# Optimization experiments

Hardware: AMD Instinct MI355X
Metric: run time of the kernel (lower is better)

## Reference

```python
import jax, jax.numpy as jnp
import numpy as np

HEADS = 4
PK = 32  # patch_kernel


def _starts(size, step, d):
    out = []
    for i in range(0, size + step - d, step):
        out.append(min(i, size - d))
    return np.asarray(out)


def dwconv3(x, w, b=None):
    # depthwise 3x3 conv, NCHW, weight (C,1,3,3)
    y = jax.lax.conv_general_dilated(
        x, w, window_strides=(1, 1), padding=((1, 1), (1, 1)),
        dimension_numbers=("NCHW", "OIHW", "NCHW"), feature_group_count=x.shape[1])
    if b is not None:
        y = y + b[None, :, None, None]
    return y


def conv1(x, w):
    # 1x1 conv as channel matmul, weight (O, C)
    return jnp.einsum("bchw,oc->bohw", x, w)


def partition(x, step, d):
    # overlapping windows, matching local_partition (i outer, j inner)
    b, c, h, w = x.shape
    sh = _starts(h, step, d)
    sw = _starts(w, step, d)
    ridx = sh[:, None] + np.arange(d)            # (nh, d)
    cidx = sw[:, None] + np.arange(d)            # (nw, d)
    xw = x[:, :, ridx, :]                        # (b, c, nh, d, w)
    xw = xw[:, :, :, :, cidx]                    # (b, c, nh, d, nw, d)
    xw = jnp.transpose(xw, (0, 2, 4, 1, 3, 5))   # (b, nh, nw, c, d, d)
    return xw.reshape(b, len(sh) * len(sw), c, d, d)


def reverse(shape, win, step, d):
    # overlap-add + count-based averaging, matching local_reverse
    b, c, h, w = shape
    sh = _starts(h, step, d)
    sw = _starts(w, step, d)
    nh, nw = len(sh), len(sw)
    ridx = (sh[:, None] + np.arange(d)).reshape(nh, 1, d, 1)
    cidx = (sw[:, None] + np.arange(d)).reshape(1, nw, 1, d)
    win6 = win.reshape(b, nh, nw, c, d, d).transpose(0, 3, 1, 2, 4, 5)  # (b,c,nh,nw,d,d)
    out = jnp.zeros(shape, win.dtype).at[:, :, ridx, cidx].add(win6)
    cnt = jnp.zeros((h, w), win.dtype).at[ridx, cidx].add(1.0)
    return out / cnt[None, None]


def setup_inputs() -> dict:
    key = jax.random.key(0)
    ks = jax.random.split(key, 9)
    b, dim, Hs, Hx = 2, 128, 62, 248
    s = 0.05
    return {
        "x": jax.random.normal(ks[0], (b, dim, Hx, Hx), jnp.float32),
        "sp": jax.random.normal(ks[1], (b, dim, Hs, Hs), jnp.float32),
        "w_pos": jax.random.normal(ks[2], (dim, 1, 3, 3), jnp.float32) * s,
        "b_pos": jax.random.normal(ks[3], (dim,), jnp.float32) * s,
        "w_q": jax.random.normal(ks[4], (dim, dim), jnp.float32) * s,
        "w_qdw": jax.random.normal(ks[5], (dim, 1, 3, 3), jnp.float32) * s,
        "w_kv": jax.random.normal(ks[6], (2 * dim, dim), jnp.float32) * s,
        "w_kvdw": jax.random.normal(ks[7], (2 * dim, 1, 3, 3), jnp.float32) * s,
        "w_out": jax.random.normal(ks[8], (dim, dim), jnp.float32) * s,
    }


def reference(x, sp, w_pos, b_pos, w_q, w_qdw, w_kv, w_kvdw, w_out):
    p1, p2 = PK, PK // 4               # 32, 8
    s1, s2 = p1 - p1 // 4, p2 - p2 // 4  # 24, 6
    x = x + dwconv3(x, w_pos, b_pos)
    sp = sp + dwconv3(sp, w_pos, b_pos)
    q = dwconv3(conv1(sp, w_q), w_qdw)      # (b, c, Hs, Ws)
    kv = dwconv3(conv1(x, w_kv), w_kvdw)    # (b, 2c, Hx, Wx)
    qw = partition(q, s2, p2)               # (b, n, c, 8, 8)
    kvw = partition(kv, s1, p1)             # (b, n, 2c, 32, 32)
    kw, vw = jnp.split(kvw, 2, axis=2)
    b, n, c = qw.shape[0], qw.shape[1], qw.shape[2]
    hd = c // HEADS

    def to_heads(t, d):  # 'b n (head c) dh dw -> (b n) head (dh dw) c'
        return t.reshape(b * n, HEADS, hd, d * d).transpose(0, 1, 3, 2)

    qh, kh, vh = to_heads(qw, p2), to_heads(kw, p1), to_heads(vw, p1)
    attn = jax.nn.softmax(jnp.einsum("bhqc,bhkc->bhqk", qh, kh) * (hd ** -0.5), axis=-1)
    out = jnp.einsum("bhqk,bhkc->bhqc", attn, vh)
    out = out.transpose(0, 1, 3, 2).reshape(b, n, c, p2, p2)
    out = reverse(sp.shape, out, s2, p2)
    return conv1(out, w_out)
```

## Files before the change

### kernel.cpp

```cpp
#include <hip/hip_runtime.h>
#include <cstdint>

#define HS 62
#define HX 248
#define HXW (HX * HX)
#define HSW (HS * HS)
#define HXP 256
#define HXWP (HX * HXP)

typedef __attribute__((ext_vector_type(8))) short bf16x8;
typedef __attribute__((ext_vector_type(4))) float f32x4;
typedef __attribute__((ext_vector_type(2))) float f32x2;

static __device__ __forceinline__ unsigned short f2bf(float f) {
  uint32_t u = __builtin_bit_cast(uint32_t, f);
  u += 0x7fff + ((u >> 16) & 1);
  return (unsigned short)(u >> 16);
}
static __device__ __forceinline__ float bf2f(unsigned short u) {
  uint32_t x = (uint32_t)u << 16;
  return __builtin_bit_cast(float, x);
}
static __device__ __forceinline__ float bflo(uint32_t u) {
  return __builtin_bit_cast(float, u << 16);
}
static __device__ __forceinline__ float bfhi(uint32_t u) {
  return __builtin_bit_cast(float, u & 0xffff0000u);
}

static __device__ __forceinline__ void pkfma(f32x2& acc, f32x2 a, f32x2 b) {
  asm("v_pk_fma_f32 %0, %1, %2, %0" : "+v"(acc) : "v"(a), "v"(b));
}
static __device__ __forceinline__ uint32_t cvtpk(float lo, float hi) {
  uint32_t r;
  asm("v_cvt_pk_bf16_f32 %0, %1, %2" : "=v"(r) : "v"(lo), "v"(hi));
  return r;
}
static __device__ __forceinline__ f32x2 unp(uint32_t u) {
  f32x2 r;
  r.x = __builtin_bit_cast(float, u << 16);
  r.y = __builtin_bit_cast(float, u & 0xffff0000u);
  return r;
}

__global__ void dwconv3_kernel(const float* __restrict__ x, const float* __restrict__ w,
                               const float* __restrict__ bias, float* __restrict__ y,
                               int C, int H, int W, int total, int residual) {
  int i = blockIdx.x * 256 + threadIdx.x;
  if (i >= total) return;
  int wx = i % W;
  int t = i / W;
  int hy = t % H;
  int bc = t / H;
  int c = bc % C;
  const float* xb = x + (size_t)bc * H * W;
  const float* wc = w + c * 9;
  float s = bias ? bias[c] : 0.0f;
  for (int di = -1; di <= 1; di++) {
    int h2 = hy + di;
    if (h2 < 0 || h2 >= H) continue;
    for (int dj = -1; dj <= 1; dj++) {
      int w2 = wx + dj;
      if (w2 < 0 || w2 >= W) continue;
      s += xb[(size_t)h2 * W + w2] * wc[(di + 1) * 3 + (dj + 1)];
    }
  }
  if (residual) s += xb[(size_t)hy * W + wx];
  y[i] = s;
}

__global__ __launch_bounds__(256) void dwconv8x2_bf16_kernel(
    const float* __restrict__ x, const float* __restrict__ w,
    const float* __restrict__ bias, unsigned short* __restrict__ y, int total) {
  int i = blockIdx.x * 256 + threadIdx.x;
  if (i >= total) return;
  int wq = (i % 31) * 8;
  int t = i / 31;
  int hp = t % 124;
  int bc = t / 124;
  int c = bc & 127;
  int hy = hp * 2;
  const float* xb = x + (size_t)bc * HXW;
  const float* wc = w + c * 9;
  float bv = bias[c];

  float rm1[10], r0[10], r1[10], r2[10];
  auto loadrow = [&](int h2, float (&r)[10]) {
    const float* row = xb + (size_t)h2 * HX + wq;
    float4 a = *(const float4*)row;
    float4 b2 = *(const float4*)(row + 4);
    r[1] = a.x;  r[2] = a.y;  r[3] = a.z;  r[4] = a.w;
    r[5] = b2.x; r[6] = b2.y; r[7] = b2.z; r[8] = b2.w;
    r[0] = (wq > 0) ? row[-1] : 0.0f;
    r[9] = (wq + 8 < HX) ? row[8] : 0.0f;
  };
  loadrow((hy > 0) ? hy - 1 : 0, rm1);
  loadrow(hy, r0);
  loadrow(hy + 1, r1);
  loadrow((hy + 2 < HX) ? hy + 2 : HX - 1, r2);
  if (hp == 0) {
#pragma unroll
    for (int k = 0; k < 10; k++) rm1[k] = 0.0f;
  }
  if (hp == 123) {
#pragma unroll
    for (int k = 0; k < 10; k++) r2[k] = 0.0f;
  }

  float w0 = wc[0], w1 = wc[1], w2 = wc[2];
  float w3 = wc[3], w4 = wc[4], w5 = wc[5];
  float w6 = wc[6], w7 = wc[7], w8 = wc[8];

  float o0[8], o1[8];
#pragma unroll
  for (int k = 0; k < 8; k++) {
    float s = bv;
    s += w0 * rm1[k]; s += w1 * rm1[k + 1]; s += w2 * rm1[k + 2];
    s += w3 * r0[k];  s += w4 * r0[k + 1];  s += w5 * r0[k + 2];
    s += w6 * r1[k];  s += w7 * r1[k + 1];  s += w8 * r1[k + 2];
    o0[k] = s + r0[k + 1];
    float u = bv;
    u += w0 * r0[k]; u += w1 * r0[k + 1]; u += w2 * r0[k + 2];
    u += w3 * r1[k]; u += w4 * r1[k + 1]; u += w5 * r1[k + 2];
    u += w6 * r2[k]; u += w7 * r2[k + 1]; u += w8 * r2[k + 2];
    o1[k] = u + r1[k + 1];
  }
  uint4 d0, d1;
  d0.x = cvtpk(o0[0], o0[1]); d0.y = cvtpk(o0[2], o0[3]);
  d0.z = cvtpk(o0[4], o0[5]); d0.w = cvtpk(o0[6], o0[7]);
  d1.x = cvtpk(o1[0], o1[1]); d1.y = cvtpk(o1[2], o1[3]);
  d1.z = cvtpk(o1[4], o1[5]); d1.w = cvtpk(o1[6], o1[7]);
  unsigned short* yb = y + (size_t)bc * HXW + (size_t)hy * HX + wq;
  *(uint4*)yb = d0;
  *(uint4*)(yb + HX) = d1;
}

__global__ void cvt_bf16_kernel(const float* __restrict__ src, unsigned short* __restrict__ dst,
                                int n) {
  int i = blockIdx.x * 256 + threadIdx.x;
  if (i < n) dst[i] = f2bf(src[i]);
}

__global__ void dwconv_q_kernel(const float* __restrict__ x, const float* __restrict__ w,
                                unsigned short* __restrict__ qn, int total) {
  int i = blockIdx.x * 256 + threadIdx.x;
  if (i >= total) return;
  int wx = i % HS;
  int t = i / HS;
  int hy = t % HS;
  int bc = t / HS;
  int c = bc & 127;
  int b = bc >> 7;
  const float* xb = x + (size_t)bc * HSW;
  const float* wc = w + c * 9;
  float s = 0.0f;
  for (int di = -1; di <= 1; di++) {
    int h2 = hy + di;
    if (h2 < 0 || h2 >= HS) continue;
    for (int dj = -1; dj <= 1; dj++) {
      int w2 = wx + dj;
      if (w2 < 0 || w2 >= HS) continue;
      s += xb[(size_t)h2 * HS + w2] * wc[(di + 1) * 3 + (dj + 1)];
    }
  }
  qn[((size_t)(b * HSW + hy * HS + wx)) * 128 + c] = f2bf(s * 0.17677669529663688f);
}

__global__ __launch_bounds__(256) void conv1_kv_mfma_kernel(
    const unsigned short* __restrict__ xpb,
    const unsigned short* __restrict__ wkb,
    unsigned short* __restrict__ y) {
  int b = blockIdx.y;
  int p0 = blockIdx.x * 64;
  int tid = threadIdx.x;
  int wave = tid >> 6, lane = tid & 63, quad = lane >> 4, l15 = lane & 15;
  __shared__ __align__(16) unsigned short bufA[64 * 136];
  __shared__ __align__(16) unsigned short bufW[64 * 136];

  {
    int c = tid >> 1, half = tid & 1;
    const unsigned short* src = xpb + ((size_t)(b * 128 + c)) * HXW + p0 + half * 32;
#pragma unroll
    for (int j = 0; j < 8; j++) {
      uint2 v = *(const uint2*)(src + j * 4);
      int px = half * 32 + j * 4;
      bufA[(px + 0) * 136 + c] = (unsigned short)(v.x & 0xffff);
      bufA[(px + 1) * 136 + c] = (unsigned short)(v.x >> 16);
      bufA[(px + 2) * 136 + c] = (unsigned short)(v.y & 0xffff);
      bufA[(px + 3) * 136 + c] = (unsigned short)(v.y >> 16);
    }
  }
  __syncthreads();
  bf16x8 A[4];
#pragma unroll
  for (int kb = 0; kb < 4; kb++)
    A[kb] = __builtin_bit_cast(bf16x8,
        *(const uint4*)&bufA[(wave * 16 + l15) * 136 + kb * 32 + quad * 8]);

  const f32x4 zf = {0.f, 0.f, 0.f, 0.f};
#pragma unroll 1
  for (int h = 0; h < 2; h++) {
#pragma unroll 1
    for (int oq = 0; oq < 2; oq++) {
      __syncthreads();
      {
        int orow = tid >> 2;
        int cseg = (tid & 3) * 32;
        const unsigned short* src = wkb + (size_t)(h * 128 + oq * 64 + orow) * 128 + cseg;
        unsigned short* dst = &bufW[orow * 136 + cseg];
        *(uint4*)(dst)      = *(const uint4*)(src);
        *(uint4*)(dst + 8)  = *(const uint4*)(src + 8);
        *(uint4*)(dst + 16) = *(const uint4*)(src + 16);
        *(uint4*)(dst + 24) = *(const uint4*)(src + 24);
      }
      __syncthreads();
#pragma unroll
      for (int ot = 0; ot < 4; ot++) {
        const unsigned short* wrow = &bufW[(ot * 16 + l15) * 136 + quad * 8];
        f32x4 D = zf;
        D = __builtin_amdgcn_mfma_f32_16x16x32_bf16(A[0], __builtin_bit_cast(bf16x8, *(const uint4*)(wrow)),      D, 0, 0, 0);
        D = __builtin_amdgcn_mfma_f32_16x16x32_bf16(A[1], __builtin_bit_cast(bf16x8, *(const uint4*)(wrow + 32)), D, 0, 0, 0);
        D = __builtin_amdgcn_mfma_f32_16x16x32_bf16(A[2], __builtin_bit_cast(bf16x8, *(const uint4*)(wrow + 64)), D, 0, 0, 0);
        D = __builtin_amdgcn_mfma_f32_16x16x32_bf16(A[3], __builtin_bit_cast(bf16x8, *(const uint4*)(wrow + 96)), D, 0, 0, 0);
#pragma unroll
        for (int r = 0; r < 4; r++)
          bufA[(wave * 16 + quad * 4 + r) * 136 + (oq * 4 + ot) * 16 + l15] = f2bf(D[r]);
      }
    }
    __syncthreads();
    {
      int px = tid >> 2, og = (tid & 3) * 32;
      const uint4* srcp = (const uint4*)&bufA[px * 136 + og];
      uint4* dstp = (uint4*)(y + ((size_t)b * HXW + p0 + px) * 256 + h * 128 + og);
#pragma unroll
      for (int j = 0; j < 4; j++) dstp[j] = srcp[j];
    }
  }
}

template <bool VT, bool VB>
static __device__ __forceinline__ void dwkv_rowpair(
    const unsigned short* __restrict__ rm1, const unsigned short* __restrict__ r0,
    const unsigned short* __restrict__ r1, const unsigned short* __restrict__ r2,
    const f32x2 (&wp)[9], int px0, f32x2 (&a0)[8], f32x2 (&a1)[8]) {
  const f32x2 z2 = {0.f, 0.f};
#pragma unroll
  for (int p = 0; p < 8; p++) { a0[p] = z2; a1[p] = z2; }
#pragma unroll
  for (int j = 0; j < 10; j++) {
    int xcol = px0 - 1 + j;
    int xc = xcol;
    if (j == 0) xc = (xcol < 0) ? 0 : xcol;
    if (j == 9) xc = (xcol > HX - 1) ? HX - 1 : xcol;
    size_t off = (size_t)xc * 256;
    uint32_t um1 = 0, u0, u1, u2 = 0;
    u0 = *(const uint32_t*)(r0 + off);
    u1 = *(const uint32_t*)(r1 + off);
    if constexpr (VT) um1 = *(const uint32_t*)(rm1 + off);
    if constexpr (VB) u2 = *(const uint32_t*)(r2 + off);
    if (j == 0 || j == 9) {
      bool oob = (j == 0) ? (xcol < 0) : (xcol > HX - 1);
      if (oob) { um1 = 0u; u0 = 0u; u1 = 0u; u2 = 0u; }
    }
    f32x2 dm1, d0 = unp(u0), d1 = unp(u1), d2;
    if constexpr (VT) dm1 = unp(um1);
    if constexpr (VB) d2 = unp(u2);
    if (j <= 7) {
      if constexpr (VT) pkfma(a0[j], wp[0], dm1);
      pkfma(a0[j], wp[3], d0);
      pkfma(a0[j], wp[6], d1);
      pkfma(a1[j], wp[0], d0);
      pkfma(a1[j], wp[3], d1);
      if constexpr (VB) pkfma(a1[j], wp[6], d2);
    }
    if (j >= 1 && j <= 8) {
      if constexpr (VT) pkfma(a0[j - 1], wp[1], dm1);
      pkfma(a0[j - 1], wp[4], d0);
      pkfma(a0[j - 1], wp[7], d1);
      pkfma(a1[j - 1], wp[1], d0);
      pkfma(a1[j - 1], wp[4], d1);
      if constexpr (VB) pkfma(a1[j - 1], wp[7], d2);
    }
    if (j >= 2) {
      if constexpr (VT) pkfma(a0[j - 2], wp[2], dm1);
      pkfma(a0[j - 2], wp[5], d0);
      pkfma(a0[j - 2], wp[8], d1);
      pkfma(a1[j - 2], wp[2], d0);
      pkfma(a1[j - 2], wp[5], d1);
      if constexpr (VB) pkfma(a1[j - 2], wp[8], d2);
    }
  }
}

#define VTS 72
#define VTROW (128 * VTS + 16)

__global__ __launch_bounds__(512) __attribute__((amdgpu_waves_per_eu(4)))
void dwconv_kv_kernel(const unsigned short* __restrict__ tkv,
                      const float* __restrict__ w,
                      unsigned short* __restrict__ kT,
                      unsigned short* __restrict__ vv) {
  int fid = blockIdx.x;
  int xcd = fid & 7, slot = fid >> 3;
  int gi = xcd * 62 + slot;
  int strip = gi / 124;
  int g = gi % 124;
  int b = blockIdx.y;
  int x0 = strip * 64;
  int tid = threadIdx.x;
  int cl = tid & 127;
  int pg = tid >> 7;
  int ch0 = cl * 2;
  int hy0 = g * 2;

  f32x2 wp[9];
#pragma unroll
  for (int t = 0; t < 9; t++) {
    wp[t].x = w[ch0 * 9 + t];
    wp[t].y = w[(ch0 + 1) * 9 + t];
  }

  __shared__ __align__(16) unsigned short vt[2 * VTROW];

  const unsigned short* r0 = tkv + (size_t)b * HXW * 256 + (size_t)hy0 * (HX * 256) + ch0;
  const unsigned short* r1 = r0 + HX * 256;
  const unsigned short* rm1 = r0 - HX * 256;
  const unsigned short* r2 = r1 + HX * 256;
  bool isK = (cl < 64);
  int c0 = ch0 - 128;

#pragma unroll 1
  for (int half = 0; half < 2; half++) {
    int px0 = x0 + pg * 16 + half * 8;
    if (px0 < HX) {
      f32x2 a0[8], a1[8];
      if (g == 0)        dwkv_rowpair<false, true >(rm1, r0, r1, r2, wp, px0, a0, a1);
      else if (g == 123) dwkv_rowpair<true,  false>(rm1, r0, r1, r2, wp, px0, a0, a1);
      else               dwkv_rowpair<true,  true >(rm1, r0, r1, r2, wp, px0, a0, a1);

      if (isK) {
        unsigned short* kb0 = kT + ((size_t)b * HXW + (size_t)hy0 * HX + px0) * 128 + ch0;
        unsigned short* kb1 = kb0 + (size_t)HX * 128;
#pragma unroll
        for (int p = 0; p < 8; p++) {
          *(uint32_t*)(kb0 + (size_t)p * 128) = cvtpk(a0[p].x, a0[p].y);
          *(uint32_t*)(kb1 + (size_t)p * 128) = cvtpk(a1[p].x, a1[p].y);
        }
      } else {
        int pxr = pg * 16 + half * 8;
        unsigned short* v0 = vt + c0 * VTS + pxr;
        unsigned short* v1 = v0 + VTS;
        uint2 d;
        d.x = cvtpk(a0[0].x, a0[1].x); d.y = cvtpk(a0[2].x, a0[3].x);
        *(uint2*)(v0) = d;
        d.x = cvtpk(a0[4].x, a0[5].x); d.y = cvtpk(a0[6].x, a0[7].x);
        *(uint2*)(v0 + 4) = d;
        d.x = cvtpk(a0[0].y, a0[1].y); d.y = cvtpk(a0[2].y, a0[3].y);
        *(uint2*)(v1) = d;
        d.x = cvtpk(a0[4].y, a0[5].y); d.y = cvtpk(a0[6].y, a0[7].y);
        *(uint2*)(v1 + 4) = d;
        d.x = cvtpk(a1[0].x, a1[1].x); d.y = cvtpk(a1[2].x, a1[3].x);
        *(uint2*)(v0 + VTROW) = d;
        d.x = cvtpk(a1[4].x, a1[5].x); d.y = cvtpk(a1[6].x, a1[7].x);
        *(uint2*)(v0 + VTROW + 4) = d;
        d.x = cvtpk(a1[0].y, a1[1].y); d.y = cvtpk(a1[2].y, a1[3].y);
        *(uint2*)(v1 + VTROW) = d;
        d.x = cvtpk(a1[4].y, a1[5].y); d.y = cvtpk(a1[6].y, a1[7].y);
        *(uint2*)(v1 + VTROW + 4) = d;
      }
    }
  }
  __syncthreads();
  {
    int ch = tid >> 2;
    int row = (tid >> 1) & 1;
    int ph = (tid & 1) * 32;
    const unsigned short* srcv = vt + row * VTROW + ch * VTS + ph;
    unsigned short* dst = vv + (size_t)(b * 128 + ch) * HXWP + (size_t)(hy0 + row) * HXP + x0 + ph;
#pragma unroll
    for (int j = 0; j < 4; j++)
      *(uint4*)(dst + j * 8) = *(const uint4*)(srcv + j * 8);
  }
}

template <int O>
__global__ __launch_bounds__(256) void conv1_kernel(const float* __restrict__ x,
                                                    const float* __restrict__ w,
                                                    float* __restrict__ y, int HW) {
  constexpr int K = 128;
  constexpr int BK = 32;
  __shared__ __align__(16) float ws_s[BK][64];
  __shared__ __align__(16) float xs_s[BK][64];
  int b = blockIdx.z;
  int o0 = blockIdx.y * 64;
  int p0 = blockIdx.x * 64;
  const float* xb = x + (size_t)b * K * HW;
  int tx = threadIdx.x & 15;
  int ty = threadIdx.x >> 4;
  float acc[4][4] = {};
  int lo = threadIdx.x >> 2;
  int lk = (threadIdx.x & 3) * 8;
  int lc = threadIdx.x >> 3;
  int lp = (threadIdx.x & 7) * 8;

  for (int k0 = 0; k0 < K; k0 += BK) {
    __syncthreads();
    {
      const float* wp = w + (size_t)(o0 + lo) * K + k0 + lk;
      float4 a = *(const float4*)wp;
      float4 bq = *(const float4*)(wp + 4);
      ws_s[lk + 0][lo] = a.x;  ws_s[lk + 1][lo] = a.y;
      ws_s[lk + 2][lo] = a.z;  ws_s[lk + 3][lo] = a.w;
      ws_s[lk + 4][lo] = bq.x; ws_s[lk + 5][lo] = bq.y;
      ws_s[lk + 6][lo] = bq.z; ws_s[lk + 7][lo] = bq.w;
    }
    {
      int p = p0 + lp;
      const float* xp = xb + (size_t)(k0 + lc) * HW;
      float4 a, bq;
      if (p + 7 < HW) {
        a = *(const float4*)(xp + p);
        bq = *(const float4*)(xp + p + 4);
      } else {
        float tv[8];
#pragma unroll
        for (int j = 0; j < 8; j++) tv[j] = (p + j < HW) ? xp[p + j] : 0.0f;
        a = make_float4(tv[0], tv[1], tv[2], tv[3]);
        bq = make_float4(tv[4], tv[5], tv[6], tv[7]);
      }
      *(float4*)&xs_s[lc][lp] = a;
      *(float4*)&xs_s[lc][lp + 4] = bq;
    }
    __syncthreads();
#pragma unroll
    for (int k = 0; k < BK; k++) {
      float4 wv = *(const float4*)&ws_s[k][ty * 4];
      float4 xv = *(const float4*)&xs_s[k][tx * 4];
      acc[0][0] += wv.x * xv.x; acc[0][1] += wv.x * xv.y; acc[0][2] += wv.x * xv.z; acc[0][3] += wv.x * xv.w;
      acc[1][0] += wv.y * xv.x; acc[1][1] += wv.y * xv.y; acc[1][2] += wv.y * xv.z; acc[1][3] += wv.y * xv.w;
      acc[2][0] += wv.z * xv.x; acc[2][1] += wv.z * xv.y; acc[2][2] += wv.z * xv.z; acc[2][3] += wv.z * xv.w;
      acc[3][0] += wv.w * xv.x; acc[3][1] += wv.w * xv.y; acc[3][2] += wv.w * xv.z; acc[3][3] += wv.w * xv.w;
    }
  }
  int p = p0 + tx * 4;
  float* yb = y + (size_t)b * O * HW + (size_t)(o0 + ty * 4) * HW;
#pragma unroll
  for (int j = 0; j < 4; j++) {
    float* yr = yb + (size_t)j * HW + p;
    if (p + 3 < HW) {
      *(float4*)yr = make_float4(acc[j][0], acc[j][1], acc[j][2], acc[j][3]);
    } else {
#pragma unroll
      for (int e = 0; e < 4; e++) if (p + e < HW) yr[e] = acc[j][e];
    }
  }
}

__global__ __launch_bounds__(256) void attn_mfma_kernel(
    const unsigned short* __restrict__ qn,
    const unsigned short* __restrict__ kT,
    const unsigned short* __restrict__ vp,
    float* __restrict__ o) {
  int fid = blockIdx.x;
  int xcd = fid & 7, slot = fid >> 3;
  int lin = xcd * 100 + slot;
  int n = lin % 100;
  int bh = lin / 100;
  int h = bh & 3, b = bh >> 2;
  int wi = n / 10, wj = n % 10;
  int wave = threadIdx.x >> 6;
  int oct = wave;
  int lane = threadIdx.x & 63;
  int quad = lane >> 4;
  int l15 = lane & 15;
  int y0 = 24 * wi, x0 = 24 * wj;

  __shared__ __align__(16) unsigned short lds[16896];
  unsigned short* Pw = lds + wave * 2560;

  bf16x8 QB[4];
#pragma unroll
  for (int nt = 0; nt < 4; nt++) {
    int qq = nt * 16 + l15;
    int qy = 6 * wi + (qq >> 3), qx = 6 * wj + (qq & 7);
    QB[nt] = __builtin_bit_cast(bf16x8,
        *(const uint4*)(qn + ((size_t)(b * HSW + qy * HS + qx)) * 128 + h * 32 + quad * 8));
  }

  f32x4 Oacc[2][4];
#pragma unroll
  for (int a = 0; a < 2; a++)
#pragma unroll
    for (int c = 0; c < 4; c++) Oacc[a][c] = f32x4{0.f, 0.f, 0.f, 0.f};
  float lsum[4] = {0.f, 0.f, 0.f, 0.f};

  const unsigned short* kb = kT + (size_t)b * HXW * 128 + h * 32;
  const unsigned short* vb = vp + ((size_t)(b * 128 + h * 32)) * HXWP;
  const f32x4 zf = {0.f, 0.f, 0.f, 0.f};

#define LOADROW(r, K0, K1, V0, V1)                                              \
  {                                                                             \
    int y = y0 + (r);                                                           \
    const unsigned short* krow = kb + ((size_t)(y * HX + x0)) * 128;            \
    K0 = *(const uint4*)(krow + (size_t)l15 * 128 + quad * 8);                  \
    K1 = *(const uint4*)(krow + (size_t)(16 + l15) * 128 + quad * 8);           \
    const unsigned short* vrow = vb + (size_t)y * HXP + x0 + quad * 8;          \
    V0 = *(const uint4*)(vrow + (size_t)l15 * HXWP);                            \
    V1 = *(const uint4*)(vrow + (size_t)(16 + l15) * HXWP);                     \
  }

  auto compute = [&](uint4 k0, uint4 k1, uint4 v0, uint4 v1) {
    bf16x8 KA0 = __builtin_bit_cast(bf16x8, k0);
    bf16x8 KA1 = __builtin_bit_cast(bf16x8, k1);
    bf16x8 VA0 = __builtin_bit_cast(bf16x8, v0);
    bf16x8 VA1 = __builtin_bit_cast(bf16x8, v1);
    f32x4 S[2][4];
#pragma unroll
    for (int nt = 0; nt < 4; nt++) {
      S[0][nt] = __builtin_amdgcn_mfma_f32_16x16x32_bf16(KA0, QB[nt], zf, 0, 0, 0);
      S[1][nt] = __builtin_amdgcn_mfma_f32_16x16x32_bf16(KA1, QB[nt], zf, 0, 0, 0);
    }
#pragma unroll
    for (int nt = 0; nt < 4; nt++) {
      float pv[2][4];
      float cs = 0.f;
#pragma unroll
      for (int mt = 0; mt < 2; mt++)
#pragma unroll
        for (int r = 0; r < 4; r++) {
          pv[mt][r] = __expf(S[mt][nt][r]);
          cs += pv[mt][r];
        }
      lsum[nt] += cs;
#pragma unroll
      for (int mt = 0; mt < 2; mt++) {
        uint2 d;
        d.x = (uint32_t)f2bf(pv[mt][0]) | ((uint32_t)f2bf(pv[mt][1]) << 16);
        d.y = (uint32_t)f2bf(pv[mt][2]) | ((uint32_t)f2bf(pv[mt][3]) << 16);
        *(uint2*)(Pw + (16 * nt + l15) * 40 + 16 * mt + quad * 4) = d;
      }
    }
#pragma unroll
    for (int nt = 0; nt < 4; nt++) {
      bf16x8 PB = __builtin_bit_cast(bf16x8, *(const uint4*)(Pw + (16 * nt + l15) * 40 + quad * 8));
      Oacc[0][nt] = __builtin_amdgcn_mfma_f32_16x16x32_bf16(VA0, PB, Oacc[0][nt], 0, 0, 0);
      Oacc[1][nt] = __builtin_amdgcn_mfma_f32_16x16x32_bf16(VA1, PB, Oacc[1][nt], 0, 0, 0);
    }
  };

  int rbase = oct * 8;
  uint4 kA0, kA1, vA0, vA1, kB0, kB1, vB0, vB1;
  LOADROW(rbase + 0, kA0, kA1, vA0, vA1);
  LOADROW(rbase + 1, kB0, kB1, vB0, vB1);
#pragma unroll 1
  for (int r = 0; r < 8; r += 2) {
    compute(kA0, kA1, vA0, vA1);
    {
      int rn = (r + 2 < 8) ? (r + 2) : 6;
      LOADROW(rbase + rn, kA0, kA1, vA0, vA1);
    }
    compute(kB0, kB1, vB0, vB1);
    {
      int rn = (r + 3 < 8) ? (r + 3) : 7;
      LOADROW(rbase + rn, kB0, kB1, vB0, vB1);
    }
  }
#undef LOADROW

#pragma unroll
  for (int nt = 0; nt < 4; nt++) {
    lsum[nt] += __shfl_xor(lsum[nt], 16, 64);
    lsum[nt] += __shfl_xor(lsum[nt], 32, 64);
  }

  float* mO = (float*)lds;
  float* mL = (float*)(lds + 16384);
  __syncthreads();
#pragma unroll
  for (int mt = 0; mt < 2; mt++)
#pragma unroll
    for (int nt = 0; nt < 4; nt++)
#pragma unroll
      for (int r = 0; r < 4; r++)
        mO[oct * 2048 + (16 * mt + quad * 4 + r) * 64 + 16 * nt + l15] = Oacc[mt][nt][r];
  if (quad == 0) {
#pragma unroll
    for (int nt = 0; nt < 4; nt++) mL[oct * 64 + nt * 16 + l15] = lsum[nt];
  }
  __syncthreads();
  {
    int q = threadIdx.x & 63;
    int cg = threadIdx.x >> 6;
    float inv = 1.0f / (mL[q] + mL[64 + q] + mL[128 + q] + mL[192 + q]);
    float* ob = o + (((size_t)(b * 100 + n)) * 128 + h * 32 + cg * 8) * 64 + q;
#pragma unroll
    for (int e = 0; e < 8; e++) {
      int ch = cg * 8 + e;
      float s = mO[ch * 64 + q] + mO[2048 + ch * 64 + q] +
                mO[4096 + ch * 64 + q] + mO[6144 + ch * 64 + q];
      ob[(size_t)e * 64] = s * inv;
    }
  }
}

__global__ void reverse_kernel(const float* __restrict__ win, float* __restrict__ out) {
  int i = blockIdx.x * 256 + threadIdx.x;
  const int total = 2 * 128 * HSW;
  if (i >= total) return;
  int x = i % HS;
  int t = i / HS;
  int y = t % HS;
  t /= HS;
  int c = t % 128;
  int b = t / 128;
  int wi0 = (y >= 7) ? (y - 2) / 6 : 0;
  int wi1 = min(9, y / 6);
  int wj0 = (x >= 7) ? (x - 2) / 6 : 0;
  int wj1 = min(9, x / 6);
  float s = 0.0f;
  for (int wi = wi0; wi <= wi1; wi++)
    for (int wj = wj0; wj <= wj1; wj++) {
      int di = y - 6 * wi, dj = x - 6 * wj;
      s += win[(((size_t)(b * 100 + wi * 10 + wj)) * 128 + c) * 64 + di * 8 + dj];
    }
  float cnt = (float)((wi1 - wi0 + 1) * (wj1 - wj0 + 1));
  out[i] = s / cnt;
}

extern "C" void kernel_launch(void* const* d_in, const int* in_sizes, int n_in,
                              void* d_out, int out_size, void* d_ws, size_t ws_size,
                              hipStream_t stream) {
  const float* x      = (const float*)d_in[0];
  const float* sp     = (const float*)d_in[1];
  const float* w_pos  = (const float*)d_in[2];
  const float* b_pos  = (const float*)d_in[3];
  const float* w_q    = (const float*)d_in[4];
  const float* w_qdw  = (const float*)d_in[5];
  const float* w_kv   = (const float*)d_in[6];
  const float* w_kvdw = (const float*)d_in[7];
  const float* w_out  = (const float*)d_in[8];
  float* out = (float*)d_out;

  const size_t N_x   = (size_t)2 * 128 * HXW;
  const size_t N_vp  = (size_t)2 * 128 * HXWP;
  const size_t N_s   = (size_t)2 * 128 * HSW;
  const size_t N_att = (size_t)2 * 100 * 128 * 64;

  float* ws = (float*)d_ws;
  unsigned short* xpb = (unsigned short*)ws;
  unsigned short* kT  = (unsigned short*)ws;
  unsigned short* vv  = kT + N_x;
  unsigned short* tkv = vv + N_vp;
  float* att = (float*)tkv;
  float* rev = att + N_att;
  float* spp = (float*)(tkv + 2 * N_x);
  float* tq  = spp + N_s;
  unsigned short* qn  = (unsigned short*)(tq + N_s);
  unsigned short* wkb = qn + N_s;
  (void)ws_size; (void)in_sizes; (void)n_in; (void)out_size;

  cvt_bf16_kernel<<<128, 256, 0, stream>>>(w_kv, wkb, 256 * 128);
  {
    int total = 2 * 128 * 124 * 31;
    dwconv8x2_bf16_kernel<<<(total + 255) / 256, 256, 0, stream>>>(x, w_pos, b_pos, xpb, total);
  }
  {
    int total = (int)N_s;
    dwconv3_kernel<<<(total + 255) / 256, 256, 0, stream>>>(sp, w_pos, b_pos, spp, 128, HS, HS, total, 1);
  }
  {
    int HW = HSW;
    dim3 grid((HW + 63) / 64, 2, 2);
    conv1_kernel<128><<<grid, 256, 0, stream>>>(spp, w_q, tq, HW);
  }
  {
    int total = (int)N_s;
    dwconv_q_kernel<<<(total + 255) / 256, 256, 0, stream>>>(tq, w_qdw, qn, total);
  }
  {
    dim3 grid(HXW / 64, 2);
    conv1_kv_mfma_kernel<<<grid, 256, 0, stream>>>(xpb, wkb, tkv);
  }
  {
    dim3 grid(496, 2);
    dwconv_kv_kernel<<<grid, 512, 0, stream>>>(tkv, w_kvdw, kT, vv);
  }
  {
    attn_mfma_kernel<<<800, 256, 0, stream>>>(qn, kT, vv, att);
  }
  {
    int total = (int)N_s;
    reverse_kernel<<<(total + 255) / 256, 256, 0, stream>>>(att, rev);
  }
  {
    int HW = HSW;
    dim3 grid((HW + 63) / 64, 2, 2);
    conv1_kernel<128><<<grid, 256, 0, stream>>>(rev, w_out, out, HW);
  }
}
```

Baseline: 257.1 us.

## Prepack kv weights into MFMA fragments and stream them from global in conv1_kv

A new kernel packs w_kv into bf16 in per-lane MFMA B-fragment order, replacing the plain float-to-bf16 conversion. The conv1_kv kernel now reads B fragments straight from global memory into registers with one-step prefetch, instead of staging weights through a shared buffer with barriers. The input transpose into shared memory uses vectorised 16-byte loads, packs four channels per store, and uses an XOR swizzle to reduce bank conflicts. This cuts shared memory and barriers, in exchange for more global/L2 weight traffic per block and extra register pressure.

```diff
diff --git a/kernel.cpp b/kernel.cpp
--- a/kernel.cpp
+++ b/kernel.cpp
@@ -135,10 +135,18 @@
   *(uint4*)(yb + HX) = d1;
 }
 
-__global__ void cvt_bf16_kernel(const float* __restrict__ src, unsigned short* __restrict__ dst,
-                                int n) {
+__global__ void pack_wfrag_kernel(const float* __restrict__ w_kv,
+                                  unsigned short* __restrict__ wf) {
   int i = blockIdx.x * 256 + threadIdx.x;
-  if (i < n) dst[i] = f2bf(src[i]);
+  if (i >= 4096) return;
+  int lane = i & 63;
+  int f = i >> 6;
+  int hq = f >> 4, ot = (f >> 2) & 3, kb = f & 3;
+  int l15 = lane & 15, quad = lane >> 4;
+  const float* src = w_kv + (size_t)(hq * 64 + ot * 16 + l15) * 128 + kb * 32 + quad * 8;
+  unsigned short* dst = wf + (size_t)i * 8;
+#pragma unroll
+  for (int j = 0; j < 8; j++) dst[j] = f2bf(src[j]);
 }
 
 __global__ void dwconv_q_kernel(const float* __restrict__ x, const float* __restrict__ w,
@@ -168,73 +176,95 @@
 
 __global__ __launch_bounds__(256) void conv1_kv_mfma_kernel(
     const unsigned short* __restrict__ xpb,
-    const unsigned short* __restrict__ wkb,
+    const unsigned short* __restrict__ wf,
     unsigned short* __restrict__ y) {
   int b = blockIdx.y;
   int p0 = blockIdx.x * 64;
   int tid = threadIdx.x;
   int wave = tid >> 6, lane = tid & 63, quad = lane >> 4, l15 = lane & 15;
   __shared__ __align__(16) unsigned short bufA[64 * 136];
-  __shared__ __align__(16) unsigned short bufW[64 * 136];
-
-  {
-    int c = tid >> 1, half = tid & 1;
-    const unsigned short* src = xpb + ((size_t)(b * 128 + c)) * HXW + p0 + half * 32;
-#pragma unroll
-    for (int j = 0; j < 8; j++) {
-      uint2 v = *(const uint2*)(src + j * 4);
-      int px = half * 32 + j * 4;
-      bufA[(px + 0) * 136 + c] = (unsigned short)(v.x & 0xffff);
-      bufA[(px + 1) * 136 + c] = (unsigned short)(v.x >> 16);
-      bufA[(px + 2) * 136 + c] = (unsigned short)(v.y & 0xffff);
-      bufA[(px + 3) * 136 + c] = (unsigned short)(v.y >> 16);
+
+  {
+    int pxg = (tid & 7) * 8;
+    int c0 = (tid >> 3) * 4;
+    const unsigned short* src = xpb + ((size_t)(b * 128 + c0)) * HXW + p0 + pxg;
+    uint4 r0 = *(const uint4*)(src);
+    uint4 r1 = *(const uint4*)(src + (size_t)HXW);
+    uint4 r2 = *(const uint4*)(src + 2 * (size_t)HXW);
+    uint4 r3 = *(const uint4*)(src + 3 * (size_t)HXW);
+    const uint32_t* q0 = (const uint32_t*)&r0;
+    const uint32_t* q1 = (const uint32_t*)&r1;
+    const uint32_t* q2 = (const uint32_t*)&r2;
+    const uint32_t* q3 = (const uint32_t*)&r3;
+    int swz = ((pxg >> 3) & 7) << 3;
+    int cs = c0 ^ swz;
+#pragma unroll
+    for (int p = 0; p < 4; p++) {
+      uint32_t d0 = q0[p], d1 = q1[p], d2 = q2[p], d3 = q3[p];
+      uint2 wlo, whi;
+      wlo.x = (d0 & 0xffffu) | (d1 << 16);
+      wlo.y = (d2 & 0xffffu) | (d3 << 16);
+      whi.x = (d0 >> 16) | (d1 & 0xffff0000u);
+      whi.y = (d2 >> 16) | (d3 & 0xffff0000u);
+      *(uint2*)&bufA[(pxg + 2 * p) * 136 + cs] = wlo;
+      *(uint2*)&bufA[(pxg + 2 * p + 1) * 136 + cs] = whi;
     }
   }
   __syncthreads();
+
   bf16x8 A[4];
-#pragma unroll
-  for (int kb = 0; kb < 4; kb++)
-    A[kb] = __builtin_bit_cast(bf16x8,
-        *(const uint4*)&bufA[(wave * 16 + l15) * 136 + kb * 32 + quad * 8]);
+  {
+    int px = wave * 16 + l15;
+    int swz = ((px >> 3) & 7) << 3;
+#pragma unroll
+    for (int kb = 0; kb < 4; kb++)
+      A[kb] = __builtin_bit_cast(bf16x8,
+          *(const uint4*)&bufA[px * 136 + ((kb * 32 + quad * 8) ^ swz)]);
+  }
 
   const f32x4 zf = {0.f, 0.f, 0.f, 0.f};
+  const uint4* wfu = (const uint4*)wf;
+  uint4 Bc[4], Bn[4];
+  {
+    const uint4* fb = wfu + lane;
+    Bc[0] = fb[0]; Bc[1] = fb[64]; Bc[2] = fb[128]; Bc[3] = fb[192];
+  }
+  int orow = wave * 16 + quad * 4;
 #pragma unroll 1
   for (int h = 0; h < 2; h++) {
-#pragma unroll 1
-    for (int oq = 0; oq < 2; oq++) {
-      __syncthreads();
-      {
-        int orow = tid >> 2;
-        int cseg = (tid & 3) * 32;
-        const unsigned short* src = wkb + (size_t)(h * 128 + oq * 64 + orow) * 128 + cseg;
-        unsigned short* dst = &bufW[orow * 136 + cseg];
-        *(uint4*)(dst)      = *(const uint4*)(src);
-        *(uint4*)(dst + 8)  = *(const uint4*)(src + 8);
-        *(uint4*)(dst + 16) = *(const uint4*)(src + 16);
-        *(uint4*)(dst + 24) = *(const uint4*)(src + 24);
+#pragma unroll
+    for (int tt = 0; tt < 8; tt++) {
+      int t = h * 8 + tt;
+      if (t < 15) {
+        const uint4* fb = wfu + (size_t)(t + 1) * 256 + lane;
+        Bn[0] = fb[0]; Bn[1] = fb[64]; Bn[2] = fb[128]; Bn[3] = fb[192];
       }
-      __syncthreads();
-#pragma unroll
-      for (int ot = 0; ot < 4; ot++) {
-        const unsigned short* wrow = &bufW[(ot * 16 + l15) * 136 + quad * 8];
-        f32x4 D = zf;
-        D = __builtin_amdgcn_mfma_f32_16x16x32_bf16(A[0], __builtin_bit_cast(bf16x8, *(const uint4*)(wrow)),      D, 0, 0, 0);
-        D = __builtin_amdgcn_mfma_f32_16x16x32_bf16(A[1], __builtin_bit_cast(bf16x8, *(const uint4*)(wrow + 32)), D, 0, 0, 0);
-        D = __builtin_amdgcn_mfma_f32_16x16x32_bf16(A[2], __builtin_bit_cast(bf16x8, *(const uint4*)(wrow + 64)), D, 0, 0, 0);
-        D = __builtin_amdgcn_mfma_f32_16x16x32_bf16(A[3], __builtin_bit_cast(bf16x8, *(const uint4*)(wrow + 96)), D, 0, 0, 0);
-#pragma unroll
-        for (int r = 0; r < 4; r++)
-          bufA[(wave * 16 + quad * 4 + r) * 136 + (oq * 4 + ot) * 16 + l15] = f2bf(D[r]);
+      f32x4 D = zf;
+      D = __builtin_amdgcn_mfma_f32_16x16x32_bf16(A[0], __builtin_bit_cast(bf16x8, Bc[0]), D, 0, 0, 0);
+      D = __builtin_amdgcn_mfma_f32_16x16x32_bf16(A[1], __builtin_bit_cast(bf16x8, Bc[1]), D, 0, 0, 0);
+      D = __builtin_amdgcn_mfma_f32_16x16x32_bf16(A[2], __builtin_bit_cast(bf16x8, Bc[2]), D, 0, 0, 0);
+      D = __builtin_amdgcn_mfma_f32_16x16x32_bf16(A[3], __builtin_bit_cast(bf16x8, Bc[3]), D, 0, 0, 0);
+      int col = tt * 16 + l15;
+#pragma unroll
+      for (int r = 0; r < 4; r++) {
+        int row = orow + r;
+        bufA[row * 136 + (col ^ (((row >> 3) & 7) << 3))] = f2bf(D[r]);
+      }
+      if (t < 15) {
+#pragma unroll
+        for (int k = 0; k < 4; k++) Bc[k] = Bn[k];
       }
     }
     __syncthreads();
     {
       int px = tid >> 2, og = (tid & 3) * 32;
-      const uint4* srcp = (const uint4*)&bufA[px * 136 + og];
+      int swz = ((px >> 3) & 7) << 3;
       uint4* dstp = (uint4*)(y + ((size_t)b * HXW + p0 + px) * 256 + h * 128 + og);
 #pragma unroll
-      for (int j = 0; j < 4; j++) dstp[j] = srcp[j];
-    }
+      for (int j = 0; j < 4; j++)
+        dstp[j] = *(const uint4*)&bufA[px * 136 + ((og + j * 8) ^ swz)];
+    }
+    __syncthreads();
   }
 }
 
@@ -659,7 +689,7 @@
   unsigned short* wkb = qn + N_s;
   (void)ws_size; (void)in_sizes; (void)n_in; (void)out_size;
 
-  cvt_bf16_kernel<<<128, 256, 0, stream>>>(w_kv, wkb, 256 * 128);
+  pack_wfrag_kernel<<<16, 256, 0, stream>>>(w_kv, wkb);
   {
     int total = 2 * 128 * 124 * 31;
     dwconv8x2_bf16_kernel<<<(total + 255) / 256, 256, 0, stream>>>(x, w_pos, b_pos, xpb, total);
```

After: 258.5 us. Within noise of the previous version (+0.5%).

## Merge independent pre-attention kernels into three combined multi-role launches

Applied to the files above, without the earlier changes.

Independent stages are packed into three launches: the x and sp depthwise convs plus the weight conversion, the kv and q 1x1 convs, and the kv and q depthwise convs. Each launch splits its block range between roles, which removes launch gaps and lets small q-path work fill the device alongside the larger x-path kernels. The cost is shared launch bounds and shared memory sized for the largest role. comboC also runs the q dwconv at 512 threads per block under waves_per_eu(4), which may restrict its occupancy.

```diff
diff --git a/kernel.cpp b/kernel.cpp
--- a/kernel.cpp
+++ b/kernel.cpp
@@ -21,12 +21,6 @@
   uint32_t x = (uint32_t)u << 16;
   return __builtin_bit_cast(float, x);
 }
-static __device__ __forceinline__ float bflo(uint32_t u) {
-  return __builtin_bit_cast(float, u << 16);
-}
-static __device__ __forceinline__ float bfhi(uint32_t u) {
-  return __builtin_bit_cast(float, u & 0xffff0000u);
-}
 
 static __device__ __forceinline__ void pkfma(f32x2& acc, f32x2 a, f32x2 b) {
   asm("v_pk_fma_f32 %0, %1, %2, %0" : "+v"(acc) : "v"(a), "v"(b));
@@ -43,37 +37,11 @@
   return r;
 }
 
-__global__ void dwconv3_kernel(const float* __restrict__ x, const float* __restrict__ w,
-                               const float* __restrict__ bias, float* __restrict__ y,
-                               int C, int H, int W, int total, int residual) {
-  int i = blockIdx.x * 256 + threadIdx.x;
-  if (i >= total) return;
-  int wx = i % W;
-  int t = i / W;
-  int hy = t % H;
-  int bc = t / H;
-  int c = bc % C;
-  const float* xb = x + (size_t)bc * H * W;
-  const float* wc = w + c * 9;
-  float s = bias ? bias[c] : 0.0f;
-  for (int di = -1; di <= 1; di++) {
-    int h2 = hy + di;
-    if (h2 < 0 || h2 >= H) continue;
-    for (int dj = -1; dj <= 1; dj++) {
-      int w2 = wx + dj;
-      if (w2 < 0 || w2 >= W) continue;
-      s += xb[(size_t)h2 * W + w2] * wc[(di + 1) * 3 + (dj + 1)];
-    }
-  }
-  if (residual) s += xb[(size_t)hy * W + wx];
-  y[i] = s;
-}
-
-__global__ __launch_bounds__(256) void dwconv8x2_bf16_kernel(
-    const float* __restrict__ x, const float* __restrict__ w,
-    const float* __restrict__ bias, unsigned short* __restrict__ y, int total) {
-  int i = blockIdx.x * 256 + threadIdx.x;
-  if (i >= total) return;
+
+static __device__ void dwconv8x2_body(const float* __restrict__ x,
+                                      const float* __restrict__ w,
+                                      const float* __restrict__ bias,
+                                      unsigned short* __restrict__ y, int i) {
   int wq = (i % 31) * 8;
   int t = i / 31;
   int hp = t % 124;
@@ -135,16 +103,34 @@
   *(uint4*)(yb + HX) = d1;
 }
 
-__global__ void cvt_bf16_kernel(const float* __restrict__ src, unsigned short* __restrict__ dst,
-                                int n) {
-  int i = blockIdx.x * 256 + threadIdx.x;
-  if (i < n) dst[i] = f2bf(src[i]);
-}
-
-__global__ void dwconv_q_kernel(const float* __restrict__ x, const float* __restrict__ w,
-                                unsigned short* __restrict__ qn, int total) {
-  int i = blockIdx.x * 256 + threadIdx.x;
-  if (i >= total) return;
+static __device__ void dwconv3sp_body(const float* __restrict__ x,
+                                      const float* __restrict__ w,
+                                      const float* __restrict__ bias,
+                                      float* __restrict__ y, int i) {
+  int wx = i % HS;
+  int t = i / HS;
+  int hy = t % HS;
+  int bc = t / HS;
+  int c = bc & 127;
+  const float* xb = x + (size_t)bc * HSW;
+  const float* wc = w + c * 9;
+  float s = bias[c];
+  for (int di = -1; di <= 1; di++) {
+    int h2 = hy + di;
+    if (h2 < 0 || h2 >= HS) continue;
+    for (int dj = -1; dj <= 1; dj++) {
+      int w2 = wx + dj;
+      if (w2 < 0 || w2 >= HS) continue;
+      s += xb[(size_t)h2 * HS + w2] * wc[(di + 1) * 3 + (dj + 1)];
+    }
+  }
+  s += xb[(size_t)hy * HS + wx];
+  y[i] = s;
+}
+
+static __device__ void dwconv_q_body(const float* __restrict__ x,
+                                     const float* __restrict__ w,
+                                     unsigned short* __restrict__ qn, int i) {
   int wx = i % HS;
   int t = i / HS;
   int hy = t % HS;
@@ -166,16 +152,15 @@
   qn[((size_t)(b * HSW + hy * HS + wx)) * 128 + c] = f2bf(s * 0.17677669529663688f);
 }
 
-__global__ __launch_bounds__(256) void conv1_kv_mfma_kernel(
-    const unsigned short* __restrict__ xpb,
-    const unsigned short* __restrict__ wkb,
-    unsigned short* __restrict__ y) {
-  int b = blockIdx.y;
-  int p0 = blockIdx.x * 64;
+static __device__ void conv1_kv_body(const unsigned short* __restrict__ xpb,
+                                     const unsigned short* __restrict__ wkb,
+                                     unsigned short* __restrict__ y,
+                                     int bx, int b, char* smem) {
+  unsigned short* bufA = (unsigned short*)smem;
+  unsigned short* bufW = bufA + 64 * 136;
+  int p0 = bx * 64;
   int tid = threadIdx.x;
   int wave = tid >> 6, lane = tid & 63, quad = lane >> 4, l15 = lane & 15;
-  __shared__ __align__(16) unsigned short bufA[64 * 136];
-  __shared__ __align__(16) unsigned short bufW[64 * 136];
 
   {
     int c = tid >> 1, half = tid & 1;
@@ -238,6 +223,79 @@
   }
 }
 
+static __device__ void conv1_body(const float* __restrict__ x,
+                                  const float* __restrict__ w,
+                                  float* __restrict__ y, int HW, int O,
+                                  int bx, int by, int bz, char* smem) {
+  constexpr int K = 128;
+  constexpr int BK = 32;
+  float (*ws_s)[64] = (float(*)[64])smem;
+  float (*xs_s)[64] = (float(*)[64])(smem + BK * 64 * sizeof(float));
+  int b = bz;
+  int o0 = by * 64;
+  int p0 = bx * 64;
+  const float* xb = x + (size_t)b * K * HW;
+  int tx = threadIdx.x & 15;
+  int ty = threadIdx.x >> 4;
+  float acc[4][4] = {};
+  int lo = threadIdx.x >> 2;
+  int lk = (threadIdx.x & 3) * 8;
+  int lc = threadIdx.x >> 3;
+  int lp = (threadIdx.x & 7) * 8;
+
+  for (int k0 = 0; k0 < K; k0 += BK) {
+    __syncthreads();
+    {
+      const float* wp = w + (size_t)(o0 + lo) * K + k0 + lk;
+      float4 a = *(const float4*)wp;
+      float4 bq = *(const float4*)(wp + 4);
+      ws_s[lk + 0][lo] = a.x;  ws_s[lk + 1][lo] = a.y;
+      ws_s[lk + 2][lo] = a.z;  ws_s[lk + 3][lo] = a.w;
+      ws_s[lk + 4][lo] = bq.x; ws_s[lk + 5][lo] = bq.y;
+      ws_s[lk + 6][lo] = bq.z; ws_s[lk + 7][lo] = bq.w;
+    }
+    {
+      int p = p0 + lp;
+      const float* xp = xb + (size_t)(k0 + lc) * HW;
+      float4 a, bq;
+      if (p + 7 < HW) {
+        a = *(const float4*)(xp + p);
+        bq = *(const float4*)(xp + p + 4);
+      } else {
+        float tv[8];
+#pragma unroll
+        for (int j = 0; j < 8; j++) tv[j] = (p + j < HW) ? xp[p + j] : 0.0f;
+        a = make_float4(tv[0], tv[1], tv[2], tv[3]);
+        bq = make_float4(tv[4], tv[5], tv[6], tv[7]);
+      }
+      *(float4*)&xs_s[lc][lp] = a;
+      *(float4*)&xs_s[lc][lp + 4] = bq;
+    }
+    __syncthreads();
+#pragma unroll
+    for (int k = 0; k < BK; k++) {
+      float4 wv = *(const float4*)&ws_s[k][ty * 4];
+      float4 xv = *(const float4*)&xs_s[k][tx * 4];
+      acc[0][0] += wv.x * xv.x; acc[0][1] += wv.x * xv.y; acc[0][2] += wv.x * xv.z; acc[0][3] += wv.x * xv.w;
+      acc[1][0] += wv.y * xv.x; acc[1][1] += wv.y * xv.y; acc[1][2] += wv.y * xv.z; acc[1][3] += wv.y * xv.w;
+      acc[2][0] += wv.z * xv.x; acc[2][1] += wv.z * xv.y; acc[2][2] += wv.z * xv.z; acc[2][3] += wv.z * xv.w;
+      acc[3][0] += wv.w * xv.x; acc[3][1] += wv.w * xv.y; acc[3][2] += wv.w * xv.z; acc[3][3] += wv.w * xv.w;
+    }
+  }
+  int p = p0 + tx * 4;
+  float* yb = y + (size_t)b * O * HW + (size_t)(o0 + ty * 4) * HW;
+#pragma unroll
+  for (int j = 0; j < 4; j++) {
+    float* yr = yb + (size_t)j * HW + p;
+    if (p + 3 < HW) {
+      *(float4*)yr = make_float4(acc[j][0], acc[j][1], acc[j][2], acc[j][3]);
+    } else {
+#pragma unroll
+      for (int e = 0; e < 4; e++) if (p + e < HW) yr[e] = acc[j][e];
+    }
+  }
+}
+
 template <bool VT, bool VB>
 static __device__ __forceinline__ void dwkv_rowpair(
     const unsigned short* __restrict__ rm1, const unsigned short* __restrict__ r0,
@@ -295,17 +353,15 @@
 #define VTS 72
 #define VTROW (128 * VTS + 16)
 
-__global__ __launch_bounds__(512) __attribute__((amdgpu_waves_per_eu(4)))
-void dwconv_kv_kernel(const unsigned short* __restrict__ tkv,
-                      const float* __restrict__ w,
-                      unsigned short* __restrict__ kT,
-                      unsigned short* __restrict__ vv) {
-  int fid = blockIdx.x;
+static __device__ void dwconv_kv_body(const unsigned short* __restrict__ tkv,
+                                      const float* __restrict__ w,
+                                      unsigned short* __restrict__ kT,
+                                      unsigned short* __restrict__ vv,
+                                      int fid, int b, unsigned short* vt) {
   int xcd = fid & 7, slot = fid >> 3;
   int gi = xcd * 62 + slot;
   int strip = gi / 124;
   int g = gi % 124;
-  int b = blockIdx.y;
   int x0 = strip * 64;
   int tid = threadIdx.x;
   int cl = tid & 127;
@@ -319,8 +375,6 @@
     wp[t].x = w[ch0 * 9 + t];
     wp[t].y = w[(ch0 + 1) * 9 + t];
   }
-
-  __shared__ __align__(16) unsigned short vt[2 * VTROW];
 
   const unsigned short* r0 = tkv + (size_t)b * HXW * 256 + (size_t)hy0 * (HX * 256) + ch0;
   const unsigned short* r1 = r0 + HX * 256;
@@ -383,77 +437,64 @@
   }
 }
 
-template <int O>
-__global__ __launch_bounds__(256) void conv1_kernel(const float* __restrict__ x,
-                                                    const float* __restrict__ w,
-                                                    float* __restrict__ y, int HW) {
-  constexpr int K = 128;
-  constexpr int BK = 32;
-  __shared__ __align__(16) float ws_s[BK][64];
-  __shared__ __align__(16) float xs_s[BK][64];
-  int b = blockIdx.z;
-  int o0 = blockIdx.y * 64;
-  int p0 = blockIdx.x * 64;
-  const float* xb = x + (size_t)b * K * HW;
-  int tx = threadIdx.x & 15;
-  int ty = threadIdx.x >> 4;
-  float acc[4][4] = {};
-  int lo = threadIdx.x >> 2;
-  int lk = (threadIdx.x & 3) * 8;
-  int lc = threadIdx.x >> 3;
-  int lp = (threadIdx.x & 7) * 8;
-
-  for (int k0 = 0; k0 < K; k0 += BK) {
-    __syncthreads();
-    {
-      const float* wp = w + (size_t)(o0 + lo) * K + k0 + lk;
-      float4 a = *(const float4*)wp;
-      float4 bq = *(const float4*)(wp + 4);
-      ws_s[lk + 0][lo] = a.x;  ws_s[lk + 1][lo] = a.y;
-      ws_s[lk + 2][lo] = a.z;  ws_s[lk + 3][lo] = a.w;
-      ws_s[lk + 4][lo] = bq.x; ws_s[lk + 5][lo] = bq.y;
-      ws_s[lk + 6][lo] = bq.z; ws_s[lk + 7][lo] = bq.w;
-    }
-    {
-      int p = p0 + lp;
-      const float* xp = xb + (size_t)(k0 + lc) * HW;
-      float4 a, bq;
-      if (p + 7 < HW) {
-        a = *(const float4*)(xp + p);
-        bq = *(const float4*)(xp + p + 4);
-      } else {
-        float tv[8];
-#pragma unroll
-        for (int j = 0; j < 8; j++) tv[j] = (p + j < HW) ? xp[p + j] : 0.0f;
-        a = make_float4(tv[0], tv[1], tv[2], tv[3]);
-        bq = make_float4(tv[4], tv[5], tv[6], tv[7]);
-      }
-      *(float4*)&xs_s[lc][lp] = a;
-      *(float4*)&xs_s[lc][lp + 4] = bq;
-    }
-    __syncthreads();
-#pragma unroll
-    for (int k = 0; k < BK; k++) {
-      float4 wv = *(const float4*)&ws_s[k][ty * 4];
-      float4 xv = *(const float4*)&xs_s[k][tx * 4];
-      acc[0][0] += wv.x * xv.x; acc[0][1] += wv.x * xv.y; acc[0][2] += wv.x * xv.z; acc[0][3] += wv.x * xv.w;
-      acc[1][0] += wv.y * xv.x; acc[1][1] += wv.y * xv.y; acc[1][2] += wv.y * xv.z; acc[1][3] += wv.y * xv.w;
-      acc[2][0] += wv.z * xv.x; acc[2][1] += wv.z * xv.y; acc[2][2] += wv.z * xv.z; acc[2][3] += wv.z * xv.w;
-      acc[3][0] += wv.w * xv.x; acc[3][1] += wv.w * xv.y; acc[3][2] += wv.w * xv.z; acc[3][3] += wv.w * xv.w;
-    }
-  }
-  int p = p0 + tx * 4;
-  float* yb = y + (size_t)b * O * HW + (size_t)(o0 + ty * 4) * HW;
-#pragma unroll
-  for (int j = 0; j < 4; j++) {
-    float* yr = yb + (size_t)j * HW + p;
-    if (p + 3 < HW) {
-      *(float4*)yr = make_float4(acc[j][0], acc[j][1], acc[j][2], acc[j][3]);
-    } else {
-#pragma unroll
-      for (int e = 0; e < 4; e++) if (p + e < HW) yr[e] = acc[j][e];
-    }
-  }
+#define NB_DW8 3844
+#define NB_DW3 3844
+#define NB_CVT 128
+
+__global__ __launch_bounds__(256) void comboA_kernel(
+    const float* __restrict__ x, const float* __restrict__ w_pos,
+    const float* __restrict__ b_pos, unsigned short* __restrict__ xpb,
+    const float* __restrict__ sp, float* __restrict__ spp,
+    const float* __restrict__ w_kv, unsigned short* __restrict__ wkb) {
+  int bid = blockIdx.x, tid = threadIdx.x;
+  if (bid < NB_DW8) {
+    int i = bid * 256 + tid;
+    dwconv8x2_body(x, w_pos, b_pos, xpb, i);
+  } else if (bid < NB_DW8 + NB_DW3) {
+    int i = (bid - NB_DW8) * 256 + tid;
+    dwconv3sp_body(sp, w_pos, b_pos, spp, i);
+  } else {
+    int i = (bid - NB_DW8 - NB_DW3) * 256 + tid;
+    if (i < 32768) wkb[i] = f2bf(w_kv[i]);
+  }
+}
+
+__global__ __launch_bounds__(256) void comboB_kernel(
+    const unsigned short* __restrict__ xpb, const unsigned short* __restrict__ wkb,
+    unsigned short* __restrict__ tkv,
+    const float* __restrict__ spp, const float* __restrict__ w_q,
+    float* __restrict__ tq) {
+  __shared__ __align__(16) char smem[64 * 136 * 2 * 2];
+  int bid = blockIdx.x;
+  if (bid < 1922) {
+    conv1_kv_body(xpb, wkb, tkv, bid % 961, bid / 961, smem);
+  } else {
+    int cid = bid - 1922;
+    conv1_body(spp, w_q, tq, HSW, 128, cid % 61, (cid / 61) % 2, cid / 122, smem);
+  }
+}
+
+__global__ __launch_bounds__(512) __attribute__((amdgpu_waves_per_eu(4)))
+void comboC_kernel(const unsigned short* __restrict__ tkv,
+                   const float* __restrict__ w_kvdw,
+                   unsigned short* __restrict__ kT, unsigned short* __restrict__ vv,
+                   const float* __restrict__ tq, const float* __restrict__ w_qdw,
+                   unsigned short* __restrict__ qn) {
+  __shared__ __align__(16) unsigned short vt[2 * VTROW];
+  int bid = blockIdx.x;
+  if (bid < 992) {
+    dwconv_kv_body(tkv, w_kvdw, kT, vv, bid % 496, bid / 496, vt);
+  } else {
+    int i = (bid - 992) * 512 + threadIdx.x;
+    if (i < 2 * 128 * HSW) dwconv_q_body(tq, w_qdw, qn, i);
+  }
+}
+
+__global__ __launch_bounds__(256) void conv1_out_kernel(const float* __restrict__ x,
+                                                        const float* __restrict__ w,
+                                                        float* __restrict__ y, int HW) {
+  __shared__ __align__(16) char smem[2 * 32 * 64 * 4];
+  conv1_body(x, w, y, HW, 128, blockIdx.x, blockIdx.y, blockIdx.z, smem);
 }
 
 __global__ __launch_bounds__(256) void attn_mfma_kernel(
@@ -659,42 +700,17 @@
   unsigned short* wkb = qn + N_s;
   (void)ws_size; (void)in_sizes; (void)n_in; (void)out_size;
 
-  cvt_bf16_kernel<<<128, 256, 0, stream>>>(w_kv, wkb, 256 * 128);
-  {
-    int total = 2 * 128 * 124 * 31;
-    dwconv8x2_bf16_kernel<<<(total + 255) / 256, 256, 0, stream>>>(x, w_pos, b_pos, xpb, total);
-  }
-  {
-    int total = (int)N_s;
-    dwconv3_kernel<<<(total + 255) / 256, 256, 0, stream>>>(sp, w_pos, b_pos, spp, 128, HS, HS, total, 1);
-  }
-  {
-    int HW = HSW;
-    dim3 grid((HW + 63) / 64, 2, 2);
-    conv1_kernel<128><<<grid, 256, 0, stream>>>(spp, w_q, tq, HW);
-  }
-  {
-    int total = (int)N_s;
-    dwconv_q_kernel<<<(total + 255) / 256, 256, 0, stream>>>(tq, w_qdw, qn, total);
-  }
-  {
-    dim3 grid(HXW / 64, 2);
-    conv1_kv_mfma_kernel<<<grid, 256, 0, stream>>>(xpb, wkb, tkv);
-  }
-  {
-    dim3 grid(496, 2);
-    dwconv_kv_kernel<<<grid, 512, 0, stream>>>(tkv, w_kvdw, kT, vv);
-  }
-  {
-    attn_mfma_kernel<<<800, 256, 0, stream>>>(qn, kT, vv, att);
-  }
+  comboA_kernel<<<NB_DW8 + NB_DW3 + NB_CVT, 256, 0, stream>>>(
+      x, w_pos, b_pos, xpb, sp, spp, w_kv, wkb);
+  comboB_kernel<<<1922 + 244, 256, 0, stream>>>(xpb, wkb, tkv, spp, w_q, tq);
+  comboC_kernel<<<992 + 1922, 512, 0, stream>>>(tkv, w_kvdw, kT, vv, tq, w_qdw, qn);
+  attn_mfma_kernel<<<800, 256, 0, stream>>>(qn, kT, vv, att);
   {
     int total = (int)N_s;
     reverse_kernel<<<(total + 255) / 256, 256, 0, stream>>>(att, rev);
   }
   {
-    int HW = HSW;
-    dim3 grid((HW + 63) / 64, 2, 2);
-    conv1_kernel<128><<<grid, 256, 0, stream>>>(rev, w_out, out, HW);
-  }
-}
+    dim3 grid((HSW + 63) / 64, 2, 2);
+    conv1_out_kernel<<<grid, 256, 0, stream>>>(rev, w_out, out, HSW);
+  }
+}
```

Measured after the change: 252.0 us. -2.0%, faster.
